# Performance work log

Measured on AMD Instinct MI355X. Metric: run time of the kernel, lower is better.

Reference implementation:

```python
import jax, jax.numpy as jnp
import numpy as np

B, N, N_IN, N_HID, N_OUT, T = 64, 64, 64, 256, 64, 4
E = N * (N - 1)  # 4032 directed edges, fully connected minus self-loops


def _incidence():
    # off-diagonal sender/receiver index pairs, NRI-style one-hot matrices
    send_idx, rec_idx = [], []
    for i in range(N):
        for j in range(N):
            if i != j:
                send_idx.append(i)
                rec_idx.append(j)
    eye = np.eye(N, dtype=np.float32)
    rel_send = eye[np.array(send_idx)]  # [E, N]
    rel_rec = eye[np.array(rec_idx)]    # [E, N]
    return jnp.asarray(rel_rec), jnp.asarray(rel_send)


def setup_inputs() -> dict:
    key = jax.random.key(0)
    ks = jax.random.split(key, 16)
    rel_rec, rel_send = _incidence()
    s1 = 1.0 / np.sqrt(2 * N_IN)
    s2 = 1.0 / np.sqrt(N_HID)
    s3 = 1.0 / np.sqrt(N_IN + N_OUT)
    return {
        "x": jax.random.normal(ks[0], (B, N, N_IN), jnp.float32),
        "rel_type": jax.random.uniform(ks[1], (B, E, T), jnp.float32),
        "rel_rec": rel_rec,
        "rel_send": rel_send,
        # per-edge-type message MLPs, stored as [T, in, out] (torch Linear transposed)
        "w1": jax.random.uniform(ks[2], (T, 2 * N_IN, N_HID), jnp.float32, -s1, s1),
        "b1": jax.random.uniform(ks[3], (T, N_HID), jnp.float32, -s1, s1),
        "w2": jax.random.uniform(ks[4], (T, N_HID, N_OUT), jnp.float32, -s2, s2),
        "b2": jax.random.uniform(ks[5], (T, N_OUT), jnp.float32, -s2, s2),
        "ow1": jax.random.uniform(ks[6], (N_IN + N_OUT, N_HID), jnp.float32, -s3, s3),
        "ob1": jax.random.uniform(ks[7], (N_HID,), jnp.float32, -s3, s3),
        "ow2": jax.random.uniform(ks[8], (N_HID, N_HID), jnp.float32, -s2, s2),
        "ob2": jax.random.uniform(ks[9], (N_HID,), jnp.float32, -s2, s2),
        "ow3": jax.random.uniform(ks[10], (N_HID, N_OUT), jnp.float32, -s2, s2),
        "ob3": jax.random.uniform(ks[11], (N_OUT,), jnp.float32, -s2, s2),
    }


def reference(x, rel_type, rel_rec, rel_send, w1, b1, w2, b2, ow1, ob1, ow2, ob2, ow3, ob3):
    # node2edge gather: [E,N] @ [B,N,F] -> [B,E,F]
    receivers = jnp.einsum('en,bnf->bef', rel_rec, x)
    senders = jnp.einsum('en,bnf->bef', rel_send, x)
    pre_msg = jnp.concatenate([senders, receivers], axis=-1)  # [B,E,2F]
    all_msgs = jnp.zeros((pre_msg.shape[0], pre_msg.shape[1], w2.shape[-1]), pre_msg.dtype)
    for i in range(w1.shape[0]):  # small fixed edge_types loop (structurally distinct weights)
        m = jax.nn.relu(pre_msg @ w1[i] + b1[i])           # [B,E,H]
        m = jax.nn.relu(m @ w2[i] + b2[i])                 # [B,E,O]
        all_msgs = all_msgs + m * rel_type[:, :, i:i + 1]  # weighted accumulate
    # edge2node scatter-aggregate: [N,E] @ [B,E,O] -> [B,N,O]
    agg_msgs = jnp.einsum('en,beo->bno', rel_rec, all_msgs)
    aug = jnp.concatenate([x, agg_msgs], axis=-1)          # [B,N,F+O]
    h = jax.nn.relu(aug @ ow1 + ob1)
    h = jax.nn.relu(h @ ow2 + ob2)
    return h @ ow3 + ob3                                   # [B,N,O]
```

## Files before the change

### kernel.cpp

```cpp
#include <hip/hip_runtime.h>

typedef unsigned short u16;
typedef __attribute__((ext_vector_type(8))) _Float16 f16x8;
typedef __attribute__((ext_vector_type(2))) _Float16 f16x2;
typedef __attribute__((ext_vector_type(4))) float f32x4;

#define DEV static __device__ __forceinline__

DEV float bf2f(u16 h){ unsigned u = ((unsigned)h) << 16; return __builtin_bit_cast(float, u); }
DEV u16 f2bf(float f){ unsigned u = __builtin_bit_cast(unsigned, f); u += 0x7FFFu + ((u >> 16) & 1u); return (u16)(u >> 16); }
DEV u16 f2h(float f){ _Float16 h = (_Float16)f; return __builtin_bit_cast(u16, h); }
DEV float h2f(u16 h){ return (float)__builtin_bit_cast(_Float16, h); }

DEV f32x4 mfma16(f16x8 a, f16x8 b, f32x4 c){
  return __builtin_amdgcn_mfma_f32_16x16x32_f16(a, b, c, 0, 0, 0);
}

DEV f16x8 build_frag(uint4 s, uint4 r){
  f16x8 a = __builtin_bit_cast(f16x8, s);
  f16x8 b = __builtin_bit_cast(f16x8, r);
  f16x8 v = a + b;
  const f16x8 z = {0,0,0,0,0,0,0,0};
  return __builtin_elementwise_max(v, z);
}

#define OFF_W1T  256
#define OFF_W2T  262400
#define OFF_OW1T 393472
#define OFF_OW2T 459008
#define OFF_OW3T 590080
#define OFF_B1   622848
#define OFF_B2   624896
#define OFF_OB1  625408
#define OFF_OB2  625920
#define OFF_OB3  626432
#define OFF_XC   626688
#define OFF_RTC  1150976
#define OFF_S1   3215360
#define OFF_R1   11603968
#define OFF_AGG  19992576

__global__ void k_sniff(const u16* __restrict__ x, int* __restrict__ flag){
  int l = threadIdx.x;
  u16 u = x[2 * l];
  int e = (u >> 7) & 0xFF;
  int ok = (e >= 103 && e <= 143) ? 1 : 0;
  unsigned long long m = __ballot(ok);
  if(l == 0) *flag = (__builtin_popcountll(m) >= 40) ? 1 : 0;
}

DEV float ldin(const void* p, int i, int isbf){
  return isbf ? bf2f(((const u16*)p)[i]) : ((const float*)p)[i];
}

__global__ __launch_bounds__(256) void k_tr(const void* __restrict__ w1, const void* __restrict__ w2,
    const void* __restrict__ ow1, const void* __restrict__ ow2, const void* __restrict__ ow3,
    char* __restrict__ ws){
  const int isbf = *(const int*)ws;
  __shared__ float tile[32][33];
  int bid = blockIdx.x, tid = threadIdx.x;
  const void* src; u16* dst; int R, C, off, r0, c0;
  if(bid < 128){ int g = bid >> 5, tt = bid & 31;
    src = w1; dst = (u16*)(ws + OFF_W1T); R = 128; C = 256; off = g * 32768;
    r0 = (tt >> 3) << 5; c0 = (tt & 7) << 5;
  } else if(bid < 192){ int bb = bid - 128; int g = bb >> 4, tt = bb & 15;
    src = w2; dst = (u16*)(ws + OFF_W2T); R = 256; C = 64; off = g * 16384;
    r0 = (tt >> 1) << 5; c0 = (tt & 1) << 5;
  } else if(bid < 224){ int bb = bid - 192;
    src = ow1; dst = (u16*)(ws + OFF_OW1T); R = 128; C = 256; off = 0;
    r0 = (bb >> 3) << 5; c0 = (bb & 7) << 5;
  } else if(bid < 288){ int bb = bid - 224;
    src = ow2; dst = (u16*)(ws + OFF_OW2T); R = 256; C = 256; off = 0;
    r0 = (bb >> 3) << 5; c0 = (bb & 7) << 5;
  } else { int bb = bid - 288;
    src = ow3; dst = (u16*)(ws + OFF_OW3T); R = 256; C = 64; off = 0;
    r0 = (bb >> 1) << 5; c0 = (bb & 1) << 5;
  }
  int tx = tid & 31, ty = tid >> 5;
  #pragma unroll
  for(int p = 0; p < 4; ++p){
    int r = ty + p * 8;
    tile[r][tx] = ldin(src, off + (r0 + r) * C + c0 + tx, isbf);
  }
  __syncthreads();
  #pragma unroll
  for(int p = 0; p < 4; ++p){
    int c = ty + p * 8;
    dst[off + (c0 + c) * R + r0 + tx] = f2h(tile[tx][c]);
  }
}

__global__ __launch_bounds__(256) void k_cvt2(const void* __restrict__ x, const void* __restrict__ rt,
    const void* __restrict__ b1, const void* __restrict__ b2,
    const void* __restrict__ ob1, const void* __restrict__ ob2, const void* __restrict__ ob3,
    char* __restrict__ ws){
  const int isbf = *(const int*)ws;
  int n = blockIdx.x * 256 + threadIdx.x;
  if(n < 262144){ ((u16*)(ws+OFF_XC))[n] = f2h(ldin(x, n, isbf)); return; }
  n -= 262144;
  if(n < 1032192){ ((u16*)(ws+OFF_RTC))[n] = f2h(ldin(rt, n, isbf)); return; }
  n -= 1032192;
  if(n < 1024){ ((u16*)(ws+OFF_B1))[n] = f2h(ldin(b1, n, isbf)); return; }
  n -= 1024;
  if(n < 256){ ((u16*)(ws+OFF_B2))[n] = f2h(ldin(b2, n, isbf)); return; }
  n -= 256;
  if(n < 256){ ((u16*)(ws+OFF_OB1))[n] = f2h(ldin(ob1, n, isbf)); return; }
  n -= 256;
  if(n < 256){ ((u16*)(ws+OFF_OB2))[n] = f2h(ldin(ob2, n, isbf)); return; }
  n -= 256;
  if(n < 64){ ((u16*)(ws+OFF_OB3))[n] = f2h(ldin(ob3, n, isbf)); return; }
}

__global__ __launch_bounds__(256) void k_s1r1(const u16* __restrict__ Xc, const u16* __restrict__ W1T,
    const u16* __restrict__ B1c, u16* __restrict__ S1, u16* __restrict__ R1){
  __shared__ __align__(16) u16 sX[64][72];
  __shared__ __align__(16) u16 sW[256][72];
  const int tid = threadIdx.x, bid = blockIdx.x;
  const int b = bid & 63, th = bid >> 6, t = th >> 1, half = th & 1;
  {
    const uint4* src = (const uint4*)(Xc + b*4096);
    #pragma unroll
    for(int it=0; it<2; ++it){
      int c = tid + it*256; int row = c >> 3, col = (c & 7) * 8;
      *(uint4*)&sX[row][col] = src[c];
    }
    const u16* base = W1T + t*32768 + half*64;
    #pragma unroll
    for(int it=0; it<8; ++it){
      int c = tid + it*256; int h = c >> 3, kc = (c & 7) * 8;
      *(uint4*)&sW[h][kc] = *(const uint4*)(base + h*128 + kc);
    }
  }
  __syncthreads();
  const int wv = tid >> 6, l = tid & 63, ml = l & 15, q = l >> 4;
  const f32x4 z = {0.f,0.f,0.f,0.f};
  f32x4 acc[4][4];
  #pragma unroll
  for(int mt=0;mt<4;++mt){ acc[mt][0]=z; acc[mt][1]=z; acc[mt][2]=z; acc[mt][3]=z; }
  #pragma unroll
  for(int ks=0; ks<2; ++ks){
    const int kb = ks*32 + q*8;
    f16x8 af[4], bff[4];
    #pragma unroll
    for(int mt=0;mt<4;++mt) af[mt] = *(const f16x8*)&sX[mt*16 + ml][kb];
    #pragma unroll
    for(int nt=0;nt<4;++nt) bff[nt] = *(const f16x8*)&sW[wv*64 + nt*16 + ml][kb];
    #pragma unroll
    for(int mt=0;mt<4;++mt)
      #pragma unroll
      for(int nt=0;nt<4;++nt)
        acc[mt][nt] = mfma16(af[mt], bff[nt], acc[mt][nt]);
  }
  u16* dst = (half ? R1 : S1) + (t*64 + b)*16384;
  #pragma unroll
  for(int nt=0;nt<4;++nt){
    const int h = wv*64 + nt*16 + ml;
    const float bias = half ? h2f(B1c[t*256 + h]) : 0.0f;
    #pragma unroll
    for(int mt=0;mt<4;++mt)
      #pragma unroll
      for(int r=0;r<4;++r){
        int irow = mt*16 + q*4 + r;
        dst[irow*256 + h] = f2h(acc[mt][nt][r] + bias);
      }
  }
}

__global__ __launch_bounds__(256, 1) void k_edge(const u16* __restrict__ RTc, const u16* __restrict__ W2T,
    const u16* __restrict__ B2c, const u16* __restrict__ S1, const u16* __restrict__ R1,
    float* __restrict__ AGG){
  __shared__ float sRTa[4][16][64];
  __shared__ float sAggB[1024];
  const int tid = threadIdx.x;
  const int t = tid >> 6, l = tid & 63, ml = l & 15, q = l >> 4;
  const int b = blockIdx.x >> 2, j0 = (blockIdx.x & 3) * 16;
  #pragma unroll
  for(int it=0; it<4; ++it) sAggB[it*256 + tid] = 0.0f;
  #pragma unroll 1
  for(int jj=0; jj<16; ++jj){
    int j = j0 + jj, i = l;
    float v = 0.0f;
    if(i != j){ int e = i*63 + j - (j > i ? 1 : 0); v = h2f(RTc[(b*4032 + e)*4 + t]); }
    sRTa[t][jj][i] = v;
  }
  __syncthreads();
  f16x8 bfr[4][8];
  {
    const u16* w2t = W2T + t*16384;
    #pragma unroll
    for(int nt=0;nt<4;++nt)
      #pragma unroll
      for(int ks=0;ks<8;++ks)
        bfr[nt][ks] = *(const f16x8*)(w2t + (nt*16 + ml)*256 + ks*32 + q*8);
  }
  uint4 su[4][8];
  const u16* s1b = S1 + (t*64 + b)*16384;
  #pragma unroll
  for(int mt=0;mt<4;++mt)
    #pragma unroll
    for(int ks=0;ks<8;++ks)
      su[mt][ks] = *(const uint4*)(s1b + (mt*16 + ml)*256 + ks*32 + q*8);
  f32x4 bini[4];
  #pragma unroll
  for(int nt=0;nt<4;++nt){
    float bv = h2f(B2c[t*64 + nt*16 + ml]);
    bini[nt].x = bv; bini[nt].y = bv; bini[nt].z = bv; bini[nt].w = bv;
  }
  const u16* r1b = R1 + (t*64 + b)*16384;
  uint4 ru[8], run[8];
  #pragma unroll
  for(int ks=0;ks<8;++ks) ru[ks] = *(const uint4*)(r1b + j0*256 + ks*32 + q*8);
  #pragma unroll 1
  for(int jj=0; jj<16; ++jj){
    f32x4 rw4[4];
    #pragma unroll
    for(int mt=0;mt<4;++mt) rw4[mt] = *(const f32x4*)&sRTa[t][jj][mt*16 + q*4];
    if(jj < 15){
      const u16* r1n = r1b + (j0 + jj + 1)*256;
      #pragma unroll
      for(int ks=0;ks<8;++ks) run[ks] = *(const uint4*)(r1n + ks*32 + q*8);
    }
    f32x4 acc[4][4];
    #pragma unroll
    for(int mt=0;mt<4;++mt){
      acc[mt][0]=bini[0]; acc[mt][1]=bini[1]; acc[mt][2]=bini[2]; acc[mt][3]=bini[3];
    }
    #pragma unroll
    for(int ks=0;ks<8;++ks){
      #pragma unroll
      for(int mt=0;mt<4;++mt){
        f16x8 af = build_frag(su[mt][ks], ru[ks]);
        #pragma unroll
        for(int nt=0;nt<4;++nt) acc[mt][nt] = mfma16(af, bfr[nt][ks], acc[mt][nt]);
      }
    }
    float cs[4] = {0.f,0.f,0.f,0.f};
    #pragma unroll
    for(int mt=0;mt<4;++mt)
      #pragma unroll
      for(int nt=0;nt<4;++nt)
        #pragma unroll
        for(int r=0;r<4;++r)
          cs[nt] += fmaxf(acc[mt][nt][r], 0.0f) * rw4[mt][r];
    #pragma unroll
    for(int nt=0;nt<4;++nt)
      atomicAdd(&sAggB[jj*64 + nt*16 + ml], cs[nt]);
    #pragma unroll
    for(int ks=0;ks<8;++ks) ru[ks] = run[ks];
  }
  __syncthreads();
  float* aggb = AGG + (b*64 + j0)*64;
  #pragma unroll
  for(int it=0; it<4; ++it) aggb[it*256 + tid] = sAggB[it*256 + tid];
}

__global__ __launch_bounds__(256) void k_node(const u16* __restrict__ Xc, const float* __restrict__ AGG,
    const u16* __restrict__ OW1T, const u16* __restrict__ OB1c,
    const u16* __restrict__ OW2T, const u16* __restrict__ OB2c,
    const u16* __restrict__ OW3T, const u16* __restrict__ OB3c,
    void* __restrict__ out, const int* __restrict__ flag){
  __shared__ __align__(16) u16 sA[64][136];
  __shared__ __align__(16) u16 sH[64][264];
  __shared__ __align__(16) u16 sH2[64][264];
  __shared__ __align__(16) u16 sW[64][264];
  const int tid = threadIdx.x, bb = blockIdx.x;
  const int isbf = *flag;
  {
    const uint4* src = (const uint4*)(Xc + bb*4096);
    #pragma unroll
    for(int it=0; it<2; ++it){
      int c = tid + it*256; int row = c >> 3, col = (c & 7)*8;
      *(uint4*)&sA[row][col] = src[c];
    }
    const float* ag = AGG + bb*4096;
    #pragma unroll
    for(int it=0; it<16; ++it){
      int c = tid + it*256; int row = c >> 6, col = c & 63;
      sA[row][64 + col] = f2h(ag[c]);
    }
  }
  const int wv = tid >> 6, l = tid & 63, ml = l & 15, q = l >> 4;
  const f32x4 z = {0.f,0.f,0.f,0.f};
  __syncthreads();
  for(int nc=0; nc<4; ++nc){
    #pragma unroll
    for(int it=0; it<4; ++it){
      int c = tid + it*256; int h = c >> 4, kc = (c & 15)*8;
      *(uint4*)&sW[h][kc] = *(const uint4*)(OW1T + (nc*64 + h)*128 + kc);
    }
    __syncthreads();
    f32x4 acc[4] = {z,z,z,z};
    #pragma unroll
    for(int ks=0; ks<4; ++ks){
      int kb = ks*32 + q*8;
      f16x8 bfrag = *(const f16x8*)&sW[wv*16 + ml][kb];
      #pragma unroll
      for(int mt=0;mt<4;++mt){
        f16x8 afrag = *(const f16x8*)&sA[mt*16 + ml][kb];
        acc[mt] = mfma16(afrag, bfrag, acc[mt]);
      }
    }
    const int h = nc*64 + wv*16 + ml;
    const float bias = h2f(OB1c[h]);
    #pragma unroll
    for(int mt=0;mt<4;++mt)
      #pragma unroll
      for(int r=0;r<4;++r){
        int row = mt*16 + q*4 + r;
        sH[row][h] = f2h(fmaxf(acc[mt][r] + bias, 0.0f));
      }
    __syncthreads();
  }
  for(int nc=0; nc<4; ++nc){
    #pragma unroll
    for(int it=0; it<8; ++it){
      int c = tid + it*256; int h = c >> 5, kc = (c & 31)*8;
      *(uint4*)&sW[h][kc] = *(const uint4*)(OW2T + (nc*64 + h)*256 + kc);
    }
    __syncthreads();
    f32x4 acc[4] = {z,z,z,z};
    #pragma unroll
    for(int ks=0; ks<8; ++ks){
      int kb = ks*32 + q*8;
      f16x8 bfrag = *(const f16x8*)&sW[wv*16 + ml][kb];
      #pragma unroll
      for(int mt=0;mt<4;++mt){
        f16x8 afrag = *(const f16x8*)&sH[mt*16 + ml][kb];
        acc[mt] = mfma16(afrag, bfrag, acc[mt]);
      }
    }
    const int h = nc*64 + wv*16 + ml;
    const float bias = h2f(OB2c[h]);
    #pragma unroll
    for(int mt=0;mt<4;++mt)
      #pragma unroll
      for(int r=0;r<4;++r){
        int row = mt*16 + q*4 + r;
        sH2[row][h] = f2h(fmaxf(acc[mt][r] + bias, 0.0f));
      }
    __syncthreads();
  }
  {
    #pragma unroll
    for(int it=0; it<8; ++it){
      int c = tid + it*256; int h = c >> 5, kc = (c & 31)*8;
      *(uint4*)&sW[h][kc] = *(const uint4*)(OW3T + h*256 + kc);
    }
    __syncthreads();
    f32x4 acc[4] = {z,z,z,z};
    #pragma unroll
    for(int ks=0; ks<8; ++ks){
      int kb = ks*32 + q*8;
      f16x8 bfrag = *(const f16x8*)&sW[wv*16 + ml][kb];
      #pragma unroll
      for(int mt=0;mt<4;++mt){
        f16x8 afrag = *(const f16x8*)&sH2[mt*16 + ml][kb];
        acc[mt] = mfma16(afrag, bfrag, acc[mt]);
      }
    }
    const int o = wv*16 + ml;
    const float bias = h2f(OB3c[o]);
    #pragma unroll
    for(int mt=0;mt<4;++mt)
      #pragma unroll
      for(int r=0;r<4;++r){
        int row = mt*16 + q*4 + r;
        float v = acc[mt][r] + bias;
        int idx = bb*4096 + row*64 + o;
        if(isbf) ((u16*)out)[idx] = f2bf(v);
        else     ((float*)out)[idx] = v;
      }
  }
}

extern "C" void kernel_launch(void* const* d_in, const int* in_sizes, int n_in,
                              void* d_out, int out_size, void* d_ws, size_t ws_size,
                              hipStream_t stream){
  (void)in_sizes; (void)n_in; (void)out_size; (void)ws_size;
  char* ws = (char*)d_ws;
  u16* W1T  = (u16*)(ws + OFF_W1T);
  u16* W2T  = (u16*)(ws + OFF_W2T);
  u16* OW1T = (u16*)(ws + OFF_OW1T);
  u16* OW2T = (u16*)(ws + OFF_OW2T);
  u16* OW3T = (u16*)(ws + OFF_OW3T);
  u16* B1c  = (u16*)(ws + OFF_B1);
  u16* B2c  = (u16*)(ws + OFF_B2);
  u16* OB1c = (u16*)(ws + OFF_OB1);
  u16* OB2c = (u16*)(ws + OFF_OB2);
  u16* OB3c = (u16*)(ws + OFF_OB3);
  u16* Xc   = (u16*)(ws + OFF_XC);
  u16* RTc  = (u16*)(ws + OFF_RTC);
  u16* S1   = (u16*)(ws + OFF_S1);
  u16* R1   = (u16*)(ws + OFF_R1);
  float* AGG = (float*)(ws + OFF_AGG);

  k_sniff<<<1, 64, 0, stream>>>((const u16*)d_in[0], (int*)ws);
  k_tr<<<304, 256, 0, stream>>>(d_in[4], d_in[6], d_in[8], d_in[10], d_in[12], ws);
  k_cvt2<<<5064, 256, 0, stream>>>(d_in[0], d_in[1], d_in[5], d_in[7],
                                   d_in[9], d_in[11], d_in[13], ws);
  k_s1r1<<<512, 256, 0, stream>>>(Xc, W1T, B1c, S1, R1);
  k_edge<<<256, 256, 0, stream>>>(RTc, W2T, B2c, S1, R1, AGG);
  k_node<<<64, 256, 0, stream>>>(Xc, AGG, OW1T, OB1c, OW2T, OB2c, OW3T, OB3c, d_out, (const int*)ws);
}
```

Measured before the change: 163.9 us.

## Split k_edge output columns across two waves per edge type, stage S1 in LDS

Measured after the change: 270.5 us. 65.1% more time.

```diff
diff --git a/kernel.cpp b/kernel.cpp
--- a/kernel.cpp
+++ b/kernel.cpp
@@ -166,92 +166,100 @@
   }
 }
 
-__global__ __launch_bounds__(256, 1) void k_edge(const u16* __restrict__ RTc, const u16* __restrict__ W2T,
+__global__ __launch_bounds__(512) void k_edge(const u16* __restrict__ RTc, const u16* __restrict__ W2T,
     const u16* __restrict__ B2c, const u16* __restrict__ S1, const u16* __restrict__ R1,
     float* __restrict__ AGG){
+  __shared__ __align__(16) u16 sS1[4][64][264];
   __shared__ float sRTa[4][16][64];
   __shared__ float sAggB[1024];
   const int tid = threadIdx.x;
-  const int t = tid >> 6, l = tid & 63, ml = l & 15, q = l >> 4;
+  const int w = tid >> 6, l = tid & 63, ml = l & 15, q = l >> 4;
+  const int t = w >> 1, nh = w & 1;
   const int b = blockIdx.x >> 2, j0 = (blockIdx.x & 3) * 16;
   #pragma unroll
-  for(int it=0; it<4; ++it) sAggB[it*256 + tid] = 0.0f;
-  #pragma unroll 1
-  for(int jj=0; jj<16; ++jj){
-    int j = j0 + jj, i = l;
-    float v = 0.0f;
-    if(i != j){ int e = i*63 + j - (j > i ? 1 : 0); v = h2f(RTc[(b*4032 + e)*4 + t]); }
-    sRTa[t][jj][i] = v;
-  }
-  __syncthreads();
-  f16x8 bfr[4][8];
+  for(int it=0; it<2; ++it) sAggB[it*512 + tid] = 0.0f;
+  #pragma unroll
+  for(int tt=0; tt<4; ++tt){
+    const uint4* src = (const uint4*)(S1 + (tt*64 + b)*16384);
+    #pragma unroll
+    for(int it=0; it<4; ++it){
+      int c = tid + it*512;
+      int row = c >> 5, col8 = (c & 31) * 8;
+      *(uint4*)&sS1[tt][row][col8] = src[c];
+    }
+  }
+  if(nh == 0){
+    #pragma unroll 1
+    for(int jj=0; jj<16; ++jj){
+      int j = j0 + jj, i = l;
+      float v = 0.0f;
+      if(i != j){ int e = i*63 + j - (j > i ? 1 : 0); v = h2f(RTc[(b*4032 + e)*4 + t]); }
+      sRTa[t][jj][i] = v;
+    }
+  }
+  f16x8 bfr[2][8];
   {
-    const u16* w2t = W2T + t*16384;
-    #pragma unroll
-    for(int nt=0;nt<4;++nt)
+    const u16* w2t = W2T + t*16384 + (nh*32)*256;
+    #pragma unroll
+    for(int nt=0;nt<2;++nt)
       #pragma unroll
       for(int ks=0;ks<8;++ks)
         bfr[nt][ks] = *(const f16x8*)(w2t + (nt*16 + ml)*256 + ks*32 + q*8);
   }
-  uint4 su[4][8];
-  const u16* s1b = S1 + (t*64 + b)*16384;
-  #pragma unroll
-  for(int mt=0;mt<4;++mt)
-    #pragma unroll
-    for(int ks=0;ks<8;++ks)
-      su[mt][ks] = *(const uint4*)(s1b + (mt*16 + ml)*256 + ks*32 + q*8);
-  f32x4 bini[4];
-  #pragma unroll
-  for(int nt=0;nt<4;++nt){
-    float bv = h2f(B2c[t*64 + nt*16 + ml]);
+  f32x4 bini[2];
+  #pragma unroll
+  for(int nt=0;nt<2;++nt){
+    float bv = h2f(B2c[t*64 + nh*32 + nt*16 + ml]);
     bini[nt].x = bv; bini[nt].y = bv; bini[nt].z = bv; bini[nt].w = bv;
   }
   const u16* r1b = R1 + (t*64 + b)*16384;
-  uint4 ru[8], run[8];
-  #pragma unroll
-  for(int ks=0;ks<8;++ks) ru[ks] = *(const uint4*)(r1b + j0*256 + ks*32 + q*8);
-  #pragma unroll 1
-  for(int jj=0; jj<16; ++jj){
+  uint4 ruA[8], ruB[8];
+  #pragma unroll
+  for(int ks=0;ks<8;++ks) ruA[ks] = *(const uint4*)(r1b + j0*256 + ks*32 + q*8);
+  __syncthreads();
+  auto body = [&](int jj, uint4 (&ru)[8], uint4 (&rn)[8], bool pf){
     f32x4 rw4[4];
     #pragma unroll
     for(int mt=0;mt<4;++mt) rw4[mt] = *(const f32x4*)&sRTa[t][jj][mt*16 + q*4];
-    if(jj < 15){
+    if(pf){
       const u16* r1n = r1b + (j0 + jj + 1)*256;
       #pragma unroll
-      for(int ks=0;ks<8;++ks) run[ks] = *(const uint4*)(r1n + ks*32 + q*8);
-    }
-    f32x4 acc[4][4];
-    #pragma unroll
-    for(int mt=0;mt<4;++mt){
-      acc[mt][0]=bini[0]; acc[mt][1]=bini[1]; acc[mt][2]=bini[2]; acc[mt][3]=bini[3];
-    }
+      for(int ks=0;ks<8;++ks) rn[ks] = *(const uint4*)(r1n + ks*32 + q*8);
+    }
+    f32x4 acc[4][2];
+    #pragma unroll
+    for(int mt=0;mt<4;++mt){ acc[mt][0]=bini[0]; acc[mt][1]=bini[1]; }
     #pragma unroll
     for(int ks=0;ks<8;++ks){
       #pragma unroll
       for(int mt=0;mt<4;++mt){
-        f16x8 af = build_frag(su[mt][ks], ru[ks]);
-        #pragma unroll
-        for(int nt=0;nt<4;++nt) acc[mt][nt] = mfma16(af, bfr[nt][ks], acc[mt][nt]);
-      }
-    }
-    float cs[4] = {0.f,0.f,0.f,0.f};
-    #pragma unroll
-    for(int mt=0;mt<4;++mt)
-      #pragma unroll
-      for(int nt=0;nt<4;++nt)
+        uint4 sv = *(const uint4*)&sS1[t][mt*16 + ml][ks*32 + q*8];
+        f16x8 af = build_frag(sv, ru[ks]);
+        acc[mt][0] = mfma16(af, bfr[0][ks], acc[mt][0]);
+        acc[mt][1] = mfma16(af, bfr[1][ks], acc[mt][1]);
+      }
+    }
+    float cs[2] = {0.f, 0.f};
+    #pragma unroll
+    for(int mt=0;mt<4;++mt)
+      #pragma unroll
+      for(int nt=0;nt<2;++nt)
         #pragma unroll
         for(int r=0;r<4;++r)
           cs[nt] += fmaxf(acc[mt][nt][r], 0.0f) * rw4[mt][r];
     #pragma unroll
-    for(int nt=0;nt<4;++nt)
-      atomicAdd(&sAggB[jj*64 + nt*16 + ml], cs[nt]);
-    #pragma unroll
-    for(int ks=0;ks<8;++ks) ru[ks] = run[ks];
+    for(int nt=0;nt<2;++nt)
+      atomicAdd(&sAggB[jj*64 + nh*32 + nt*16 + ml], cs[nt]);
+  };
+  #pragma unroll 1
+  for(int jp=0; jp<8; ++jp){
+    body(2*jp,     ruA, ruB, true);
+    body(2*jp + 1, ruB, ruA, jp < 7);
   }
   __syncthreads();
   float* aggb = AGG + (b*64 + j0)*64;
   #pragma unroll
-  for(int it=0; it<4; ++it) aggb[it*256 + tid] = sAggB[it*256 + tid];
+  for(int it=0; it<2; ++it) aggb[it*512 + tid] = sAggB[it*512 + tid];
 }
 
 __global__ __launch_bounds__(256) void k_node(const u16* __restrict__ Xc, const float* __restrict__ AGG,
@@ -399,6 +407,6 @@
   k_cvt2<<<5064, 256, 0, stream>>>(d_in[0], d_in[1], d_in[5], d_in[7],
                                    d_in[9], d_in[11], d_in[13], ws);
   k_s1r1<<<512, 256, 0, stream>>>(Xc, W1T, B1c, S1, R1);
-  k_edge<<<256, 256, 0, stream>>>(RTc, W2T, B2c, S1, R1, AGG);
+  k_edge<<<256, 512, 0, stream>>>(RTc, W2T, B2c, S1, R1, AGG);
   k_node<<<64, 256, 0, stream>>>(Xc, AGG, OW1T, OB1c, OW2T, OB2c, OW3T, OB3c, d_out, (const int*)ws);
 }
```

## Stage receiver rows in LDS and process two receivers per iteration

Applied to the files above, without the earlier changes.

After: 175.9 us. 7.3% more time.

```diff
diff --git a/kernel.cpp b/kernel.cpp
--- a/kernel.cpp
+++ b/kernel.cpp
@@ -169,6 +169,7 @@
 __global__ __launch_bounds__(256, 1) void k_edge(const u16* __restrict__ RTc, const u16* __restrict__ W2T,
     const u16* __restrict__ B2c, const u16* __restrict__ S1, const u16* __restrict__ R1,
     float* __restrict__ AGG){
+  __shared__ __align__(16) u16 sR1[4][16][264];
   __shared__ float sRTa[4][16][64];
   __shared__ float sAggB[1024];
   const int tid = threadIdx.x;
@@ -176,6 +177,15 @@
   const int b = blockIdx.x >> 2, j0 = (blockIdx.x & 3) * 16;
   #pragma unroll
   for(int it=0; it<4; ++it) sAggB[it*256 + tid] = 0.0f;
+  {
+    const u16* r1b = R1 + (t*64 + b)*16384 + j0*256;
+    #pragma unroll
+    for(int it=0; it<8; ++it){
+      int c = l + it*64;
+      int row = c >> 5, col8 = (c & 31) * 8;
+      *(uint4*)&sR1[t][row][col8] = *(const uint4*)(r1b + row*256 + col8);
+    }
+  }
   #pragma unroll 1
   for(int jj=0; jj<16; ++jj){
     int j = j0 + jj, i = l;
@@ -183,7 +193,6 @@
     if(i != j){ int e = i*63 + j - (j > i ? 1 : 0); v = h2f(RTc[(b*4032 + e)*4 + t]); }
     sRTa[t][jj][i] = v;
   }
-  __syncthreads();
   f16x8 bfr[4][8];
   {
     const u16* w2t = W2T + t*16384;
@@ -206,47 +215,59 @@
     float bv = h2f(B2c[t*64 + nt*16 + ml]);
     bini[nt].x = bv; bini[nt].y = bv; bini[nt].z = bv; bini[nt].w = bv;
   }
-  const u16* r1b = R1 + (t*64 + b)*16384;
-  uint4 ru[8], run[8];
-  #pragma unroll
-  for(int ks=0;ks<8;++ks) ru[ks] = *(const uint4*)(r1b + j0*256 + ks*32 + q*8);
+  __syncthreads();
   #pragma unroll 1
-  for(int jj=0; jj<16; ++jj){
-    f32x4 rw4[4];
-    #pragma unroll
-    for(int mt=0;mt<4;++mt) rw4[mt] = *(const f32x4*)&sRTa[t][jj][mt*16 + q*4];
-    if(jj < 15){
-      const u16* r1n = r1b + (j0 + jj + 1)*256;
-      #pragma unroll
-      for(int ks=0;ks<8;++ks) run[ks] = *(const uint4*)(r1n + ks*32 + q*8);
-    }
-    f32x4 acc[4][4];
-    #pragma unroll
-    for(int mt=0;mt<4;++mt){
-      acc[mt][0]=bini[0]; acc[mt][1]=bini[1]; acc[mt][2]=bini[2]; acc[mt][3]=bini[3];
-    }
+  for(int jp=0; jp<8; ++jp){
+    const int jjA = 2*jp, jjB = 2*jp + 1;
+    f32x4 accA[4][4], accB[4][4];
+    #pragma unroll
+    for(int mt=0;mt<4;++mt)
+      #pragma unroll
+      for(int nt=0;nt<4;++nt){ accA[mt][nt] = bini[nt]; accB[mt][nt] = bini[nt]; }
     #pragma unroll
     for(int ks=0;ks<8;++ks){
-      #pragma unroll
-      for(int mt=0;mt<4;++mt){
-        f16x8 af = build_frag(su[mt][ks], ru[ks]);
+      const uint4 rA = *(const uint4*)&sR1[t][jjA][ks*32 + q*8];
+      const uint4 rB = *(const uint4*)&sR1[t][jjB][ks*32 + q*8];
+      #pragma unroll
+      for(int mt=0;mt<4;++mt){
+        f16x8 aA = build_frag(su[mt][ks], rA);
         #pragma unroll
-        for(int nt=0;nt<4;++nt) acc[mt][nt] = mfma16(af, bfr[nt][ks], acc[mt][nt]);
-      }
-    }
-    float cs[4] = {0.f,0.f,0.f,0.f};
-    #pragma unroll
-    for(int mt=0;mt<4;++mt)
+        for(int nt=0;nt<4;++nt) accA[mt][nt] = mfma16(aA, bfr[nt][ks], accA[mt][nt]);
+        f16x8 aB = build_frag(su[mt][ks], rB);
+        #pragma unroll
+        for(int nt=0;nt<4;++nt) accB[mt][nt] = mfma16(aB, bfr[nt][ks], accB[mt][nt]);
+      }
+    }
+    {
+      float cs[4] = {0.f,0.f,0.f,0.f};
+      #pragma unroll
+      for(int mt=0;mt<4;++mt){
+        const f32x4 rw4 = *(const f32x4*)&sRTa[t][jjA][mt*16 + q*4];
+        #pragma unroll
+        for(int nt=0;nt<4;++nt)
+          #pragma unroll
+          for(int r=0;r<4;++r)
+            cs[nt] += fmaxf(accA[mt][nt][r], 0.0f) * rw4[r];
+      }
       #pragma unroll
       for(int nt=0;nt<4;++nt)
+        atomicAdd(&sAggB[jjA*64 + nt*16 + ml], cs[nt]);
+    }
+    {
+      float cs[4] = {0.f,0.f,0.f,0.f};
+      #pragma unroll
+      for(int mt=0;mt<4;++mt){
+        const f32x4 rw4 = *(const f32x4*)&sRTa[t][jjB][mt*16 + q*4];
         #pragma unroll
-        for(int r=0;r<4;++r)
-          cs[nt] += fmaxf(acc[mt][nt][r], 0.0f) * rw4[mt][r];
-    #pragma unroll
-    for(int nt=0;nt<4;++nt)
-      atomicAdd(&sAggB[jj*64 + nt*16 + ml], cs[nt]);
-    #pragma unroll
-    for(int ks=0;ks<8;++ks) ru[ks] = run[ks];
+        for(int nt=0;nt<4;++nt)
+          #pragma unroll
+          for(int r=0;r<4;++r)
+            cs[nt] += fmaxf(accB[mt][nt][r], 0.0f) * rw4[r];
+      }
+      #pragma unroll
+      for(int nt=0;nt<4;++nt)
+        atomicAdd(&sAggB[jjB*64 + nt*16 + ml], cs[nt]);
+    }
   }
   __syncthreads();
   float* aggb = AGG + (b*64 + j0)*64;
```

## Fuse input conversion into consumers, drop sniff/convert kernels, split node MLP rows

Applied to the files above, without the earlier changes.

Result: faster. 155.5 us (median of 2 runs) (-5.1%).

```diff
diff --git a/kernel.cpp b/kernel.cpp
--- a/kernel.cpp
+++ b/kernel.cpp
@@ -24,39 +24,49 @@
   return __builtin_elementwise_max(v, z);
 }
 
+DEV int sniff_isbf(const void* x){
+  int l = threadIdx.x & 63;
+  u16 u = ((const u16*)x)[2 * l];
+  int e = (u >> 7) & 0xFF;
+  int ok = (e >= 103 && e <= 143) ? 1 : 0;
+  unsigned long long m = __ballot(ok);
+  return (__builtin_popcountll(m) >= 40) ? 1 : 0;
+}
+
+DEV float ldin(const void* p, int i, int isbf){
+  return isbf ? bf2f(((const u16*)p)[i]) : ((const float*)p)[i];
+}
+
+DEV unsigned pk2(float a, float b){ return (unsigned)f2h(a) | ((unsigned)f2h(b) << 16); }
+DEV unsigned pkbf(unsigned w){
+  float lo = bf2f((u16)(w & 0xffff)), hi = bf2f((u16)(w >> 16));
+  return pk2(lo, hi);
+}
+DEV uint4 ld8f16(const void* p, int g, int isbf){
+  uint4 r;
+  if(isbf){
+    uint4 v = ((const uint4*)p)[g];
+    r.x = pkbf(v.x); r.y = pkbf(v.y); r.z = pkbf(v.z); r.w = pkbf(v.w);
+  } else {
+    float4 a = ((const float4*)p)[2*g], b4 = ((const float4*)p)[2*g + 1];
+    r.x = pk2(a.x, a.y); r.y = pk2(a.z, a.w); r.z = pk2(b4.x, b4.y); r.w = pk2(b4.z, b4.w);
+  }
+  return r;
+}
+
 #define OFF_W1T  256
 #define OFF_W2T  262400
 #define OFF_OW1T 393472
 #define OFF_OW2T 459008
 #define OFF_OW3T 590080
-#define OFF_B1   622848
-#define OFF_B2   624896
-#define OFF_OB1  625408
-#define OFF_OB2  625920
-#define OFF_OB3  626432
-#define OFF_XC   626688
-#define OFF_RTC  1150976
 #define OFF_S1   3215360
 #define OFF_R1   11603968
 #define OFF_AGG  19992576
 
-__global__ void k_sniff(const u16* __restrict__ x, int* __restrict__ flag){
-  int l = threadIdx.x;
-  u16 u = x[2 * l];
-  int e = (u >> 7) & 0xFF;
-  int ok = (e >= 103 && e <= 143) ? 1 : 0;
-  unsigned long long m = __ballot(ok);
-  if(l == 0) *flag = (__builtin_popcountll(m) >= 40) ? 1 : 0;
-}
-
-DEV float ldin(const void* p, int i, int isbf){
-  return isbf ? bf2f(((const u16*)p)[i]) : ((const float*)p)[i];
-}
-
-__global__ __launch_bounds__(256) void k_tr(const void* __restrict__ w1, const void* __restrict__ w2,
-    const void* __restrict__ ow1, const void* __restrict__ ow2, const void* __restrict__ ow3,
-    char* __restrict__ ws){
-  const int isbf = *(const int*)ws;
+__global__ __launch_bounds__(256) void k_tr(const void* __restrict__ x, const void* __restrict__ w1,
+    const void* __restrict__ w2, const void* __restrict__ ow1, const void* __restrict__ ow2,
+    const void* __restrict__ ow3, char* __restrict__ ws){
+  const int isbf = sniff_isbf(x);
   __shared__ float tile[32][33];
   int bid = blockIdx.x, tid = threadIdx.x;
   const void* src; u16* dst; int R, C, off, r0, c0;
@@ -90,39 +100,18 @@
   }
 }
 
-__global__ __launch_bounds__(256) void k_cvt2(const void* __restrict__ x, const void* __restrict__ rt,
-    const void* __restrict__ b1, const void* __restrict__ b2,
-    const void* __restrict__ ob1, const void* __restrict__ ob2, const void* __restrict__ ob3,
-    char* __restrict__ ws){
-  const int isbf = *(const int*)ws;
-  int n = blockIdx.x * 256 + threadIdx.x;
-  if(n < 262144){ ((u16*)(ws+OFF_XC))[n] = f2h(ldin(x, n, isbf)); return; }
-  n -= 262144;
-  if(n < 1032192){ ((u16*)(ws+OFF_RTC))[n] = f2h(ldin(rt, n, isbf)); return; }
-  n -= 1032192;
-  if(n < 1024){ ((u16*)(ws+OFF_B1))[n] = f2h(ldin(b1, n, isbf)); return; }
-  n -= 1024;
-  if(n < 256){ ((u16*)(ws+OFF_B2))[n] = f2h(ldin(b2, n, isbf)); return; }
-  n -= 256;
-  if(n < 256){ ((u16*)(ws+OFF_OB1))[n] = f2h(ldin(ob1, n, isbf)); return; }
-  n -= 256;
-  if(n < 256){ ((u16*)(ws+OFF_OB2))[n] = f2h(ldin(ob2, n, isbf)); return; }
-  n -= 256;
-  if(n < 64){ ((u16*)(ws+OFF_OB3))[n] = f2h(ldin(ob3, n, isbf)); return; }
-}
-
-__global__ __launch_bounds__(256) void k_s1r1(const u16* __restrict__ Xc, const u16* __restrict__ W1T,
-    const u16* __restrict__ B1c, u16* __restrict__ S1, u16* __restrict__ R1){
+__global__ __launch_bounds__(256) void k_s1r1(const void* __restrict__ x, const u16* __restrict__ W1T,
+    const void* __restrict__ b1, u16* __restrict__ S1, u16* __restrict__ R1){
   __shared__ __align__(16) u16 sX[64][72];
   __shared__ __align__(16) u16 sW[256][72];
   const int tid = threadIdx.x, bid = blockIdx.x;
   const int b = bid & 63, th = bid >> 6, t = th >> 1, half = th & 1;
+  const int isbf = sniff_isbf(x);
   {
-    const uint4* src = (const uint4*)(Xc + b*4096);
     #pragma unroll
     for(int it=0; it<2; ++it){
       int c = tid + it*256; int row = c >> 3, col = (c & 7) * 8;
-      *(uint4*)&sX[row][col] = src[c];
+      *(uint4*)&sX[row][col] = ld8f16(x, b*512 + c, isbf);
     }
     const u16* base = W1T + t*32768 + half*64;
     #pragma unroll
@@ -155,7 +144,7 @@
   #pragma unroll
   for(int nt=0;nt<4;++nt){
     const int h = wv*64 + nt*16 + ml;
-    const float bias = half ? h2f(B1c[t*256 + h]) : 0.0f;
+    const float bias = half ? ldin(b1, t*256 + h, isbf) : 0.0f;
     #pragma unroll
     for(int mt=0;mt<4;++mt)
       #pragma unroll
@@ -166,21 +155,22 @@
   }
 }
 
-__global__ __launch_bounds__(256, 1) void k_edge(const u16* __restrict__ RTc, const u16* __restrict__ W2T,
-    const u16* __restrict__ B2c, const u16* __restrict__ S1, const u16* __restrict__ R1,
-    float* __restrict__ AGG){
+__global__ __launch_bounds__(256, 1) void k_edge(const void* __restrict__ x, const void* __restrict__ rt,
+    const u16* __restrict__ W2T, const void* __restrict__ b2,
+    const u16* __restrict__ S1, const u16* __restrict__ R1, float* __restrict__ AGG){
   __shared__ float sRTa[4][16][64];
   __shared__ float sAggB[1024];
   const int tid = threadIdx.x;
   const int t = tid >> 6, l = tid & 63, ml = l & 15, q = l >> 4;
   const int b = blockIdx.x >> 2, j0 = (blockIdx.x & 3) * 16;
+  const int isbf = sniff_isbf(x);
   #pragma unroll
   for(int it=0; it<4; ++it) sAggB[it*256 + tid] = 0.0f;
   #pragma unroll 1
   for(int jj=0; jj<16; ++jj){
     int j = j0 + jj, i = l;
     float v = 0.0f;
-    if(i != j){ int e = i*63 + j - (j > i ? 1 : 0); v = h2f(RTc[(b*4032 + e)*4 + t]); }
+    if(i != j){ int e = i*63 + j - (j > i ? 1 : 0); v = ldin(rt, (b*4032 + e)*4 + t, isbf); }
     sRTa[t][jj][i] = v;
   }
   __syncthreads();
@@ -203,7 +193,7 @@
   f32x4 bini[4];
   #pragma unroll
   for(int nt=0;nt<4;++nt){
-    float bv = h2f(B2c[t*64 + nt*16 + ml]);
+    float bv = ldin(b2, t*64 + nt*16 + ml, isbf);
     bini[nt].x = bv; bini[nt].y = bv; bini[nt].z = bv; bini[nt].w = bv;
   }
   const u16* r1b = R1 + (t*64 + b)*16384;
@@ -254,29 +244,28 @@
   for(int it=0; it<4; ++it) aggb[it*256 + tid] = sAggB[it*256 + tid];
 }
 
-__global__ __launch_bounds__(256) void k_node(const u16* __restrict__ Xc, const float* __restrict__ AGG,
-    const u16* __restrict__ OW1T, const u16* __restrict__ OB1c,
-    const u16* __restrict__ OW2T, const u16* __restrict__ OB2c,
-    const u16* __restrict__ OW3T, const u16* __restrict__ OB3c,
-    void* __restrict__ out, const int* __restrict__ flag){
-  __shared__ __align__(16) u16 sA[64][136];
-  __shared__ __align__(16) u16 sH[64][264];
-  __shared__ __align__(16) u16 sH2[64][264];
+__global__ __launch_bounds__(256) void k_node(const void* __restrict__ x, const float* __restrict__ AGG,
+    const u16* __restrict__ OW1T, const void* __restrict__ ob1,
+    const u16* __restrict__ OW2T, const void* __restrict__ ob2,
+    const u16* __restrict__ OW3T, const void* __restrict__ ob3,
+    void* __restrict__ out){
+  __shared__ __align__(16) u16 sA[16][136];
+  __shared__ __align__(16) u16 sH[16][264];
+  __shared__ __align__(16) u16 sH2[16][264];
   __shared__ __align__(16) u16 sW[64][264];
-  const int tid = threadIdx.x, bb = blockIdx.x;
-  const int isbf = *flag;
+  const int tid = threadIdx.x;
+  const int bb = blockIdx.x >> 2, rg = blockIdx.x & 3;
+  const int isbf = sniff_isbf(x);
   {
-    const uint4* src = (const uint4*)(Xc + bb*4096);
-    #pragma unroll
-    for(int it=0; it<2; ++it){
-      int c = tid + it*256; int row = c >> 3, col = (c & 7)*8;
-      *(uint4*)&sA[row][col] = src[c];
+    if(tid < 128){
+      int row = tid >> 3, gc = tid & 7;
+      *(uint4*)&sA[row][gc*8] = ld8f16(x, bb*512 + (rg*16 + row)*8 + gc, isbf);
     }
     const float* ag = AGG + bb*4096;
     #pragma unroll
-    for(int it=0; it<16; ++it){
+    for(int it=0; it<4; ++it){
       int c = tid + it*256; int row = c >> 6, col = c & 63;
-      sA[row][64 + col] = f2h(ag[c]);
+      sA[row][64 + col] = f2h(ag[(rg*16 + row)*64 + col]);
     }
   }
   const int wv = tid >> 6, l = tid & 63, ml = l & 15, q = l >> 4;
@@ -289,26 +278,19 @@
       *(uint4*)&sW[h][kc] = *(const uint4*)(OW1T + (nc*64 + h)*128 + kc);
     }
     __syncthreads();
-    f32x4 acc[4] = {z,z,z,z};
+    f32x4 acc = z;
     #pragma unroll
     for(int ks=0; ks<4; ++ks){
       int kb = ks*32 + q*8;
       f16x8 bfrag = *(const f16x8*)&sW[wv*16 + ml][kb];
-      #pragma unroll
-      for(int mt=0;mt<4;++mt){
-        f16x8 afrag = *(const f16x8*)&sA[mt*16 + ml][kb];
-        acc[mt] = mfma16(afrag, bfrag, acc[mt]);
-      }
+      f16x8 afrag = *(const f16x8*)&sA[ml][kb];
+      acc = mfma16(afrag, bfrag, acc);
     }
     const int h = nc*64 + wv*16 + ml;
-    const float bias = h2f(OB1c[h]);
-    #pragma unroll
-    for(int mt=0;mt<4;++mt)
-      #pragma unroll
-      for(int r=0;r<4;++r){
-        int row = mt*16 + q*4 + r;
-        sH[row][h] = f2h(fmaxf(acc[mt][r] + bias, 0.0f));
-      }
+    const float bias = ldin(ob1, h, isbf);
+    #pragma unroll
+    for(int r=0;r<4;++r)
+      sH[q*4 + r][h] = f2h(fmaxf(acc[r] + bias, 0.0f));
     __syncthreads();
   }
   for(int nc=0; nc<4; ++nc){
@@ -318,26 +300,19 @@
       *(uint4*)&sW[h][kc] = *(const uint4*)(OW2T + (nc*64 + h)*256 + kc);
     }
     __syncthreads();
-    f32x4 acc[4] = {z,z,z,z};
+    f32x4 acc = z;
     #pragma unroll
     for(int ks=0; ks<8; ++ks){
       int kb = ks*32 + q*8;
       f16x8 bfrag = *(const f16x8*)&sW[wv*16 + ml][kb];
-      #pragma unroll
-      for(int mt=0;mt<4;++mt){
-        f16x8 afrag = *(const f16x8*)&sH[mt*16 + ml][kb];
-        acc[mt] = mfma16(afrag, bfrag, acc[mt]);
-      }
+      f16x8 afrag = *(const f16x8*)&sH[ml][kb];
+      acc = mfma16(afrag, bfrag, acc);
     }
     const int h = nc*64 + wv*16 + ml;
-    const float bias = h2f(OB2c[h]);
-    #pragma unroll
-    for(int mt=0;mt<4;++mt)
-      #pragma unroll
-      for(int r=0;r<4;++r){
-        int row = mt*16 + q*4 + r;
-        sH2[row][h] = f2h(fmaxf(acc[mt][r] + bias, 0.0f));
-      }
+    const float bias = ldin(ob2, h, isbf);
+    #pragma unroll
+    for(int r=0;r<4;++r)
+      sH2[q*4 + r][h] = f2h(fmaxf(acc[r] + bias, 0.0f));
     __syncthreads();
   }
   {
@@ -347,29 +322,24 @@
       *(uint4*)&sW[h][kc] = *(const uint4*)(OW3T + h*256 + kc);
     }
     __syncthreads();
-    f32x4 acc[4] = {z,z,z,z};
+    f32x4 acc = z;
     #pragma unroll
     for(int ks=0; ks<8; ++ks){
       int kb = ks*32 + q*8;
       f16x8 bfrag = *(const f16x8*)&sW[wv*16 + ml][kb];
-      #pragma unroll
-      for(int mt=0;mt<4;++mt){
-        f16x8 afrag = *(const f16x8*)&sH2[mt*16 + ml][kb];
-        acc[mt] = mfma16(afrag, bfrag, acc[mt]);
-      }
+      f16x8 afrag = *(const f16x8*)&sH2[ml][kb];
+      acc = mfma16(afrag, bfrag, acc);
     }
     const int o = wv*16 + ml;
-    const float bias = h2f(OB3c[o]);
-    #pragma unroll
-    for(int mt=0;mt<4;++mt)
-      #pragma unroll
-      for(int r=0;r<4;++r){
-        int row = mt*16 + q*4 + r;
-        float v = acc[mt][r] + bias;
-        int idx = bb*4096 + row*64 + o;
-        if(isbf) ((u16*)out)[idx] = f2bf(v);
-        else     ((float*)out)[idx] = v;
-      }
+    const float bias = ldin(ob3, o, isbf);
+    #pragma unroll
+    for(int r=0;r<4;++r){
+      int row = rg*16 + q*4 + r;
+      float v = acc[r] + bias;
+      int idx = bb*4096 + row*64 + o;
+      if(isbf) ((u16*)out)[idx] = f2bf(v);
+      else     ((float*)out)[idx] = v;
+    }
   }
 }
 
@@ -383,22 +353,12 @@
   u16* OW1T = (u16*)(ws + OFF_OW1T);
   u16* OW2T = (u16*)(ws + OFF_OW2T);
   u16* OW3T = (u16*)(ws + OFF_OW3T);
-  u16* B1c  = (u16*)(ws + OFF_B1);
-  u16* B2c  = (u16*)(ws + OFF_B2);
-  u16* OB1c = (u16*)(ws + OFF_OB1);
-  u16* OB2c = (u16*)(ws + OFF_OB2);
-  u16* OB3c = (u16*)(ws + OFF_OB3);
-  u16* Xc   = (u16*)(ws + OFF_XC);
-  u16* RTc  = (u16*)(ws + OFF_RTC);
   u16* S1   = (u16*)(ws + OFF_S1);
   u16* R1   = (u16*)(ws + OFF_R1);
   float* AGG = (float*)(ws + OFF_AGG);
 
-  k_sniff<<<1, 64, 0, stream>>>((const u16*)d_in[0], (int*)ws);
-  k_tr<<<304, 256, 0, stream>>>(d_in[4], d_in[6], d_in[8], d_in[10], d_in[12], ws);
-  k_cvt2<<<5064, 256, 0, stream>>>(d_in[0], d_in[1], d_in[5], d_in[7],
-                                   d_in[9], d_in[11], d_in[13], ws);
-  k_s1r1<<<512, 256, 0, stream>>>(Xc, W1T, B1c, S1, R1);
-  k_edge<<<256, 256, 0, stream>>>(RTc, W2T, B2c, S1, R1, AGG);
-  k_node<<<64, 256, 0, stream>>>(Xc, AGG, OW1T, OB1c, OW2T, OB2c, OW3T, OB3c, d_out, (const int*)ws);
-}
+  k_tr<<<304, 256, 0, stream>>>(d_in[0], d_in[4], d_in[6], d_in[8], d_in[10], d_in[12], ws);
+  k_s1r1<<<512, 256, 0, stream>>>(d_in[0], W1T, d_in[5], S1, R1);
+  k_edge<<<256, 256, 0, stream>>>(d_in[0], d_in[1], W2T, d_in[7], S1, R1, AGG);
+  k_node<<<256, 256, 0, stream>>>(d_in[0], AGG, OW1T, d_in[9], OW2T, d_in[11], OW3T, d_in[13], d_out);
+}
```
